# Performance work log

Measured on AMD Instinct MI355X. Metric: run time of the kernel, lower is better.

The kernel has to match this reference:

```python
import jax, jax.numpy as jnp
import numpy as np

B, T, C = 1, 2048, 1024
H, KVH = 16, 4
D = C // H            # 64
KV = KVH * D          # 256
EPS = 1e-6
SCALE = 1.0 / np.sqrt(D)
ROPE_BASE = 10000.0


def setup_inputs() -> dict:
    key = jax.random.key(0)
    ks = jax.random.split(key, 8)
    s = 0.02
    return dict(
        x=jax.random.normal(ks[0], (B, T, C), jnp.float32),
        Wq=jax.random.normal(ks[1], (C, C), jnp.float32) * s,
        Wk=jax.random.normal(ks[2], (KV, C), jnp.float32) * s,
        Wv=jax.random.normal(ks[3], (KV, C), jnp.float32) * s,
        Wo=jax.random.normal(ks[4], (C, C), jnp.float32) * s,
        q_norm_w=jnp.ones((C,), jnp.float32),
        k_norm_w=jnp.ones((KV,), jnp.float32),
        fgate_w=jax.random.normal(ks[5], (H, C), jnp.float32) * s,
        fgate_b=jnp.zeros((H,), jnp.float32),
        weight_lambda=jax.random.normal(ks[6], (C, H), jnp.float32) * s,
    )


def _rmsnorm(x, w):
    var = jnp.mean(x * x, axis=-1, keepdims=True)
    return x * jax.lax.rsqrt(var + EPS) * w


def _rotate_half(x):
    x1, x2 = jnp.split(x, 2, axis=-1)
    return jnp.concatenate([-x2, x1], axis=-1)


def _apply_rope(q, k):
    # q: [B,H,T,D], k: [B,KVH,T,D]; position_ids = arange(T)
    inv_freq = 1.0 / (ROPE_BASE ** (jnp.arange(0, D, 2, dtype=jnp.float32) / D))
    freqs = jnp.outer(jnp.arange(T, dtype=jnp.float32), inv_freq)  # [T, D/2]
    emb = jnp.concatenate([freqs, freqs], axis=-1)                 # [T, D]
    cos = jnp.cos(emb)[None, None]                                  # [1,1,T,D]
    sin = jnp.sin(emb)[None, None]
    return q * cos + _rotate_half(q) * sin, k * cos + _rotate_half(k) * sin


def _forward(x, Wq, Wk, Wv, Wo, q_norm_w, k_norm_w, fgate_w, fgate_b, weight_lambda):
    q = _rmsnorm(x @ Wq.T, q_norm_w)          # [B,T,C]
    k = _rmsnorm(x @ Wk.T, k_norm_w)          # [B,T,KV]
    v = x @ Wv.T                              # [B,T,KV]
    q = q.reshape(B, T, H, D).transpose(0, 2, 1, 3)     # [B,H,T,D]
    k = k.reshape(B, T, KVH, D).transpose(0, 2, 1, 3)   # [B,KVH,T,D]
    v = v.reshape(B, T, KVH, D).transpose(0, 2, 1, 3)
    q, k = _apply_rope(q, k)
    # GQA: repeat_interleave kv heads
    g = H // KVH
    k = jnp.repeat(k, g, axis=1)              # [B,H,T,D]
    v = jnp.repeat(v, g, axis=1)
    # Forgetting gate (FoX): log f_t per head, with elu-based lambda scaling
    lam = jax.nn.elu(x @ weight_lambda) + 1.0            # [B,T,H]
    logit = (x @ fgate_w.T + fgate_b) * lam              # [B,T,H]
    log_f = (jax.nn.log_sigmoid(logit) / (lam + 1e-3)).transpose(0, 2, 1)  # [B,H,T]
    c = jnp.cumsum(log_f, axis=-1)                       # [B,H,T]
    bias = c[..., :, None] - c[..., None, :]             # [B,H,T,T]: sum_{t=j+1..i} log f_t
    scores = jnp.einsum('bhid,bhjd->bhij', q, k) * SCALE + bias
    causal = jnp.tril(jnp.ones((T, T), dtype=bool))
    scores = jnp.where(causal, scores, -jnp.inf)
    p = jax.nn.softmax(scores, axis=-1)
    y = jnp.einsum('bhij,bhjd->bhid', p, v)              # [B,H,T,D]
    y = y.transpose(0, 2, 1, 3).reshape(B, T, C)
    return y @ Wo.T


def reference(x, Wq, Wk, Wv, Wo, q_norm_w, k_norm_w, fgate_w, fgate_b, weight_lambda):
    return _forward(x, Wq, Wk, Wv, Wo, q_norm_w, k_norm_w, fgate_w, fgate_b, weight_lambda)
```

## Files before the change

### kernel.cpp

```cpp
#include <hip/hip_runtime.h>

typedef __bf16 bf16x8 __attribute__((ext_vector_type(8)));
typedef float f32x4 __attribute__((ext_vector_type(4)));

#define MFMA_BF16 __builtin_amdgcn_mfma_f32_16x16x32_bf16

static constexpr int T_ = 2048;
static constexpr int C_ = 1024;
static constexpr int H_ = 16;
static constexpr int KVH_ = 4;
static constexpr int D_ = 64;
static constexpr float SCALE_ = 0.125f;
static constexpr float MSHIFT_ = 10.0f;

static constexpr int UPH_ = 528;
static constexpr int W_ = H_ * UPH_;
static constexpr int CHUNK_ = 12;
static constexpr int NBLK_ = W_ / CHUNK_;

__device__ inline void cvt8(__bf16* dst, const float* src) {
  float4 a = *(const float4*)src;
  float4 b = *(const float4*)(src + 4);
  bf16x8 r;
  r[0] = (__bf16)a.x; r[1] = (__bf16)a.y; r[2] = (__bf16)a.z; r[3] = (__bf16)a.w;
  r[4] = (__bf16)b.x; r[5] = (__bf16)b.y; r[6] = (__bf16)b.z; r[7] = (__bf16)b.w;
  *(bf16x8*)dst = r;
}

__global__ __launch_bounds__(256) void cvt_kernel(
    const float* __restrict__ x,  const float* __restrict__ wq,
    const float* __restrict__ wk, const float* __restrict__ wv,
    const float* __restrict__ wo, const float* __restrict__ wl,
    __bf16* __restrict__ xb,  __bf16* __restrict__ wqb,
    __bf16* __restrict__ wkb, __bf16* __restrict__ wvb,
    __bf16* __restrict__ wob, float* __restrict__ wlT,
    float* __restrict__ zbuf)
{
  size_t i8 = ((size_t)blockIdx.x * 256 + threadIdx.x) * 8;
  if (i8 < 2097152)       cvt8(xb  + i8,            x  + i8);
  else if (i8 < 3145728)  cvt8(wqb + (i8-2097152),  wq + (i8-2097152));
  else if (i8 < 3407872)  cvt8(wkb + (i8-3145728),  wk + (i8-3145728));
  else if (i8 < 3670016)  cvt8(wvb + (i8-3407872),  wv + (i8-3407872));
  else if (i8 < 4718592)  cvt8(wob + (i8-3670016),  wo + (i8-3670016));
  else if (i8 < 4734976) {
    size_t r = i8 - 4718592;
#pragma unroll
    for (int j = 0; j < 8; ++j) {
      size_t idx = r + j;
      size_t hh = idx >> 10, c = idx & 1023;
      wlT[idx] = wl[c * 16 + hh];
    }
  } else {
    size_t z = i8 - 4734976;
    if (z < 2129920) {
      float4 zz = {0.f, 0.f, 0.f, 0.f};
      *(float4*)(zbuf + z) = zz;
      *(float4*)(zbuf + z + 4) = zz;
    }
  }
}

template <int BM>
__global__ __launch_bounds__(256) void gemm_bt_kernel(
    const __bf16* __restrict__ A, int K, int N,
    const __bf16* __restrict__ B0, int e0,
    const __bf16* __restrict__ B1, int e1,
    const __bf16* __restrict__ B2,
    float* __restrict__ outF)
{
  __shared__ __bf16 la[BM * 40];
  __shared__ __bf16 lb[128 * 40];
  const int m0 = blockIdx.y * BM;
  const int n0 = blockIdx.x * 128;
  const __bf16* Bs; int nrel;
  if (n0 < e0)      { Bs = B0; nrel = n0; }
  else if (n0 < e1) { Bs = B1; nrel = n0 - e0; }
  else              { Bs = B2; nrel = n0 - e1; }
  const int tid = threadIdx.x;
  const int arow = tid >> 2, acol = (tid & 3) * 8;
  const __bf16* ap = A  + (size_t)(m0   + arow) * K + acol;
  const __bf16* bp = Bs + (size_t)(nrel + arow) * K + acol;
  const int w = tid >> 6, lane = tid & 63, lq = lane >> 4, ln = lane & 15;
  const int wm = (w >> 1) * (BM / 2), wn = (w & 1) * 64;
  constexpr int FM = BM / 32;
  f32x4 acc[FM][4] = {};
  for (int k0 = 0; k0 < K; k0 += 32) {
    bf16x8 a0 = *(const bf16x8*)(ap + k0);
    bf16x8 a1{};
    if (BM == 128) a1 = *(const bf16x8*)(ap + (size_t)64 * K + k0);
    bf16x8 b0 = *(const bf16x8*)(bp + k0);
    bf16x8 b1 = *(const bf16x8*)(bp + (size_t)64 * K + k0);
    __syncthreads();
    *(bf16x8*)(la + arow * 40 + acol) = a0;
    if (BM == 128) *(bf16x8*)(la + (arow + 64) * 40 + acol) = a1;
    *(bf16x8*)(lb + arow * 40 + acol) = b0;
    *(bf16x8*)(lb + (arow + 64) * 40 + acol) = b1;
    __syncthreads();
    bf16x8 af[FM], bfr[4];
#pragma unroll
    for (int i = 0; i < FM; ++i)
      af[i] = *(const bf16x8*)(la + (wm + i * 16 + ln) * 40 + lq * 8);
#pragma unroll
    for (int j = 0; j < 4; ++j)
      bfr[j] = *(const bf16x8*)(lb + (wn + j * 16 + ln) * 40 + lq * 8);
#pragma unroll
    for (int i = 0; i < FM; ++i)
#pragma unroll
      for (int j = 0; j < 4; ++j)
        acc[i][j] = MFMA_BF16(af[i], bfr[j], acc[i][j], 0, 0, 0);
  }
#pragma unroll
  for (int i = 0; i < FM; ++i)
#pragma unroll
    for (int j = 0; j < 4; ++j)
#pragma unroll
      for (int r = 0; r < 4; ++r) {
        int row = m0 + wm + i * 16 + lq * 4 + r;
        int col = n0 + wn + j * 16 + ln;
        outF[(size_t)row * N + col] = acc[i][j][r];
      }
}

__global__ __launch_bounds__(256) void gates_kernel(
    const float* __restrict__ x, const float* __restrict__ fw,
    const float* __restrict__ fb, const float* __restrict__ wlT,
    float* __restrict__ logf)
{
  const int t = blockIdx.x;
  const int tid = threadIdx.x, w = tid >> 6, lane = tid & 63;
  float xv[16];
#pragma unroll
  for (int i = 0; i < 16; ++i)
    xv[i] = x[(size_t)t * C_ + i * 64 + lane];
#pragma unroll
  for (int u = 0; u < 4; ++u) {
    int h = w * 4 + u;
    float s1 = 0.f, s2 = 0.f;
#pragma unroll
    for (int i = 0; i < 16; ++i) {
      int cidx = i * 64 + lane;
      s1 += xv[i] * wlT[(size_t)h * C_ + cidx];
      s2 += xv[i] * fw[(size_t)h * C_ + cidx];
    }
    for (int m = 32; m; m >>= 1) {
      s1 += __shfl_xor(s1, m);
      s2 += __shfl_xor(s2, m);
    }
    if (lane == 0) {
      float lam = (s1 > 0.f ? s1 : expm1f(s1)) + 1.0f;
      float logit = (s2 + fb[h]) * lam;
      float ls = (logit >= 0.f) ? -log1pf(expf(-logit))
                                : (logit - log1pf(expf(logit)));
      logf[(size_t)h * T_ + t] = ls / (lam + 1e-3f);
    }
  }
}

__global__ __launch_bounds__(64) void cumsum_kernel(
    const float* __restrict__ logf, float* __restrict__ csum)
{
  const int h = blockIdx.x;
  const int lane = threadIdx.x;
  float carry = 0.f;
  for (int ch = 0; ch < T_ / 64; ++ch) {
    float v = logf[(size_t)h * T_ + ch * 64 + lane];
#pragma unroll
    for (int d = 1; d < 64; d <<= 1) {
      float tv = __shfl_up(v, d);
      if (lane >= d) v += tv;
    }
    v += carry;
    csum[(size_t)h * T_ + ch * 64 + lane] = v;
    carry = __shfl(v, 63);
  }
}

__global__ __launch_bounds__(256) void normrope_kernel(
    const float* __restrict__ qkv, const float* __restrict__ qw,
    const float* __restrict__ kw, __bf16* __restrict__ qh,
    __bf16* __restrict__ kh, __bf16* __restrict__ vh)
{
  const int t = blockIdx.x, tid = threadIdx.x;
  __shared__ float qn[1024];
  __shared__ float kn[256];
  __shared__ float red[16];
  __shared__ float rc[32], rs[32];
  if (tid < 32) {
    float fr = (float)t * exp2f((float)tid * -0.41524101186404527f);
    float sn, cs;
    sincosf(fr, &sn, &cs);
    rc[tid] = cs; rs[tid] = sn;
  }
  const float* row = qkv + (size_t)t * 1536;
  float4 q4 = *(const float4*)(row + tid * 4);
  float kvl = row[1024 + tid];
  float vvl = row[1280 + tid];
  float ssq = q4.x * q4.x + q4.y * q4.y + q4.z * q4.z + q4.w * q4.w;
  float ssk = kvl * kvl;
  const int lane = tid & 63, w = tid >> 6;
  for (int m = 32; m; m >>= 1) {
    ssq += __shfl_xor(ssq, m);
    ssk += __shfl_xor(ssk, m);
  }
  if (lane == 0) { red[w] = ssq; red[8 + w] = ssk; }
  __syncthreads();
  float sq = red[0] + red[1] + red[2] + red[3];
  float sk = red[8] + red[9] + red[10] + red[11];
  float rq = rsqrtf(sq * (1.0f / 1024.f) + 1e-6f);
  float rk = rsqrtf(sk * (1.0f / 256.f) + 1e-6f);
  qn[tid * 4 + 0] = q4.x * rq * qw[tid * 4 + 0];
  qn[tid * 4 + 1] = q4.y * rq * qw[tid * 4 + 1];
  qn[tid * 4 + 2] = q4.z * rq * qw[tid * 4 + 2];
  qn[tid * 4 + 3] = q4.w * rq * qw[tid * 4 + 3];
  kn[tid] = kvl * rk * kw[tid];
  __syncthreads();
#pragma unroll
  for (int u = 0; u < 4; ++u) {
    int cidx = tid * 4 + u;
    int hh = cidx >> 6, d = cidx & 63, i = d & 31;
    float cs = rc[i], sn = rs[i];
    float val = (d < 32) ? (qn[cidx] * cs - qn[cidx + 32] * sn)
                         : (qn[cidx] * cs + qn[cidx - 32] * sn);
    qh[(size_t)hh * T_ * D_ + (size_t)t * D_ + d] = (__bf16)val;
  }
  {
    int d = tid & 63, kvhh = tid >> 6, i = d & 31;
    float cs = rc[i], sn = rs[i];
    float kval = (d < 32) ? (kn[tid] * cs - kn[tid + 32] * sn)
                          : (kn[tid] * cs + kn[tid - 32] * sn);
    kh[(size_t)kvhh * T_ * D_ + (size_t)t * D_ + d] = (__bf16)kval;
    vh[(size_t)kvhh * T_ * D_ + (size_t)t * D_ + d] = (__bf16)vvl;
  }
}

__global__ __launch_bounds__(256) void vtrans_kernel(
    const __bf16* __restrict__ vh, __bf16* __restrict__ vt)
{
  const int tb = blockIdx.x, kvh = blockIdx.y;
  __shared__ __bf16 tile[64][72];
  const int tid = threadIdx.x;
  const int r = tid >> 2, cb = (tid & 3) * 16;
  const __bf16* src = vh + (size_t)kvh * T_ * D_ + (size_t)(tb * 64 + r) * D_ + cb;
  bf16x8 v0 = *(const bf16x8*)(src);
  bf16x8 v1 = *(const bf16x8*)(src + 8);
  *(bf16x8*)(&tile[r][cb]) = v0;
  *(bf16x8*)(&tile[r][cb + 8]) = v1;
  __syncthreads();
  bf16x8 o0, o1;
#pragma unroll
  for (int j = 0; j < 8; ++j) o0[j] = tile[cb + j][r];
#pragma unroll
  for (int j = 0; j < 8; ++j) o1[j] = tile[cb + 8 + j][r];
  __bf16* dst = vt + (size_t)kvh * D_ * T_ + (size_t)r * T_ + tb * 64 + cb;
  *(bf16x8*)(dst) = o0;
  *(bf16x8*)(dst + 8) = o1;
}

__global__ __launch_bounds__(256) void attn_kernel(
    const __bf16* __restrict__ qh, const __bf16* __restrict__ kh,
    const __bf16* __restrict__ vt, const float* __restrict__ csum,
    float* __restrict__ oacc, float* __restrict__ lsacc)
{
  const int bid = blockIdx.x;
  const int wgid = (bid & 7) * (NBLK_ / 8) + (bid >> 3);
  const int u0 = wgid * CHUNK_;
  __shared__ __bf16 kbuf[2][64 * 72];
  __shared__ __bf16 vbuf[2][64 * 72];
  __shared__ __bf16 pt[4][16 * 76];
  const int tid = threadIdx.x;
  const int w = tid >> 6, lane = tid & 63, lq = lane >> 4, ln = lane & 15;
  const int srow = tid >> 2, scol = (tid & 3) * 16;
  bf16x8 ones;
#pragma unroll
  for (int j = 0; j < 8; ++j) ones[j] = (__bf16)1.0f;
  __bf16* pw = &pt[w][0];

  auto dec = [](int u, int& h, int& ib, int& jt) {
    h = u / UPH_;
    int uh = u - h * UPH_;
    int b = (int)((sqrtf((float)(8 * uh + 1)) - 1.f) * 0.5f);
    if (b * (b + 1) / 2 > uh) --b;
    if ((b + 1) * (b + 2) / 2 <= uh) ++b;
    ib = b; jt = uh - b * (b + 1) / 2;
  };

  int h, ib, jt;
  dec(u0, h, ib, jt);
  int kvh = h >> 2;

  bf16x8 aq0, aq1;
  float ci[4];
  f32x4 o[4] = {};
  f32x4 ls = {0.f, 0.f, 0.f, 0.f};
  auto loadQ = [&](int h_, int i0_) {
    const __bf16* qp = qh + ((size_t)h_ * T_ + i0_ + w * 16 + ln) * D_;
    aq0 = *(const bf16x8*)(qp + lq * 8);
    aq1 = *(const bf16x8*)(qp + 32 + lq * 8);
#pragma unroll
    for (int r = 0; r < 4; ++r)
      ci[r] = csum[(size_t)h_ * T_ + i0_ + w * 16 + lq * 4 + r];
#pragma unroll
    for (int dd = 0; dd < 4; ++dd) o[dd] = f32x4{0.f, 0.f, 0.f, 0.f};
    ls = f32x4{0.f, 0.f, 0.f, 0.f};
  };
  loadQ(h, ib * 64);

  auto fetchRegs = [&](int kvh_, int jt_, bf16x8& k0, bf16x8& k1,
                       bf16x8& v0, bf16x8& v1) {
    const __bf16* kb = kh + (size_t)kvh_ * T_ * D_;
    const __bf16* vb = vt + (size_t)kvh_ * D_ * T_;
    k0 = *(const bf16x8*)(kb + (size_t)(jt_ * 64 + srow) * D_ + scol);
    k1 = *(const bf16x8*)(kb + (size_t)(jt_ * 64 + srow) * D_ + scol + 8);
    v0 = *(const bf16x8*)(vb + (size_t)srow * T_ + jt_ * 64 + scol);
    v1 = *(const bf16x8*)(vb + (size_t)srow * T_ + jt_ * 64 + scol + 8);
  };
  auto writeStage = [&](int cb, bf16x8 k0, bf16x8 k1, bf16x8 v0, bf16x8 v1) {
    *(bf16x8*)(kbuf[cb] + srow * 72 + scol) = k0;
    *(bf16x8*)(kbuf[cb] + srow * 72 + scol + 8) = k1;
    *(bf16x8*)(vbuf[cb] + srow * 72 + scol) = v0;
    *(bf16x8*)(vbuf[cb] + srow * 72 + scol + 8) = v1;
  };

  auto tilebody = [&](int cb, int j0, bool diag) {
    const __bf16* kt = kbuf[cb];
    const __bf16* vtt = vbuf[cb];
    float cj[4];
#pragma unroll
    for (int jj = 0; jj < 4; ++jj)
      cj[jj] = csum[(size_t)h * T_ + j0 + jj * 16 + ln];
    f32x4 s[4];
    const f32x4 zf = {0.f, 0.f, 0.f, 0.f};
#pragma unroll
    for (int jj = 0; jj < 4; ++jj) {
      bf16x8 bk0 = *(const bf16x8*)(kt + (jj * 16 + ln) * 72 + lq * 8);
      bf16x8 bk1 = *(const bf16x8*)(kt + (jj * 16 + ln) * 72 + 32 + lq * 8);
      s[jj] = MFMA_BF16(aq0, bk0, zf, 0, 0, 0);
      s[jj] = MFMA_BF16(aq1, bk1, s[jj], 0, 0, 0);
    }
    bf16x8 bv0[4], bv1[4];
#pragma unroll
    for (int dd = 0; dd < 4; ++dd) {
      bv0[dd] = *(const bf16x8*)(vtt + (dd * 16 + ln) * 72 + lq * 8);
      bv1[dd] = *(const bf16x8*)(vtt + (dd * 16 + ln) * 72 + 32 + lq * 8);
    }
#pragma unroll
    for (int jj = 0; jj < 4; ++jj)
#pragma unroll
      for (int r = 0; r < 4; ++r) {
        float arg = fmaf(s[jj][r], SCALE_, ci[r] - cj[jj] - MSHIFT_);
        float p = __expf(arg);
        if (diag && (jj * 16 + ln > w * 16 + lq * 4 + r)) p = 0.f;
        pw[(lq * 4 + r) * 76 + jj * 16 + ln] = (__bf16)p;
      }
    asm volatile("s_waitcnt lgkmcnt(0)" ::: "memory");
    bf16x8 pa0 = *(const bf16x8*)(pw + ln * 76 + lq * 8);
    bf16x8 pa1 = *(const bf16x8*)(pw + ln * 76 + 32 + lq * 8);
    ls = MFMA_BF16(pa0, ones, ls, 0, 0, 0);
    ls = MFMA_BF16(pa1, ones, ls, 0, 0, 0);
#pragma unroll
    for (int dd = 0; dd < 4; ++dd) {
      o[dd] = MFMA_BF16(pa0, bv0[dd], o[dd], 0, 0, 0);
      o[dd] = MFMA_BF16(pa1, bv1[dd], o[dd], 0, 0, 0);
    }
  };

  auto flush = [&]() {
    const int i0 = ib * 64;
#pragma unroll
    for (int dd = 0; dd < 4; ++dd)
#pragma unroll
      for (int r = 0; r < 4; ++r) {
        int iabs = i0 + w * 16 + lq * 4 + r;
        atomicAdd(oacc + ((size_t)h * T_ + iabs) * D_ + dd * 16 + ln,
                  o[dd][r]);
      }
    if (ln == 0) {
#pragma unroll
      for (int r = 0; r < 4; ++r)
        atomicAdd(lsacc + (size_t)h * T_ + ib * 64 + w * 16 + lq * 4 + r,
                  ls[r]);
    }
  };

  {
    bf16x8 k0, k1, v0, v1;
    fetchRegs(kvh, jt, k0, k1, v0, v1);
    writeStage(0, k0, k1, v0, v1);
  }
  __syncthreads();

  int cur = 0;
#pragma unroll 1
  for (int s = 0; s < CHUNK_; ++s) {
    const bool last = (s == CHUNK_ - 1);
    int nh = 0, nib = 0, njt = 0;
    bf16x8 k0, k1, v0, v1;
    if (!last) {
      dec(u0 + s + 1, nh, nib, njt);
      fetchRegs(nh >> 2, njt, k0, k1, v0, v1);
    }
    tilebody(cur, jt * 64, jt == ib);
    if (!last) writeStage(cur ^ 1, k0, k1, v0, v1);
    const bool rowEnd = last || nib != ib || nh != h;
    if (rowEnd) flush();
    if (!last) {
      __syncthreads();
      if (nh != h || nib != ib) loadQ(nh, nib * 64);
      h = nh; ib = nib; jt = njt; kvh = nh >> 2;
      cur ^= 1;
    }
  }
}

__global__ __launch_bounds__(256) void attnfin_kernel(
    const float* __restrict__ oacc, const float* __restrict__ lsacc,
    __bf16* __restrict__ y)
{
  const int t = blockIdx.x;
  const int c = threadIdx.x * 4;
  const int h = c >> 6, d = c & 63;
  float inv = 1.0f / lsacc[(size_t)h * T_ + t];
  float4 o4 = *(const float4*)(oacc + ((size_t)h * T_ + t) * D_ + d);
  __bf16* yp = y + (size_t)t * C_ + c;
  yp[0] = (__bf16)(o4.x * inv);
  yp[1] = (__bf16)(o4.y * inv);
  yp[2] = (__bf16)(o4.z * inv);
  yp[3] = (__bf16)(o4.w * inv);
}

extern "C" void kernel_launch(void* const* d_in, const int* in_sizes, int n_in,
                              void* d_out, int out_size, void* d_ws, size_t ws_size,
                              hipStream_t stream) {
  const float* x   = (const float*)d_in[0];
  const float* Wq  = (const float*)d_in[1];
  const float* Wk  = (const float*)d_in[2];
  const float* Wv  = (const float*)d_in[3];
  const float* Wo  = (const float*)d_in[4];
  const float* qnw = (const float*)d_in[5];
  const float* knw = (const float*)d_in[6];
  const float* fgw = (const float*)d_in[7];
  const float* fgb = (const float*)d_in[8];
  const float* wl  = (const float*)d_in[9];

  char* ws = (char*)d_ws;
  size_t off = 0;
  float*  qkv  = (float*)(ws + off);  off += (size_t)T_ * 1536 * 4;
  float*  logf = (float*)(ws + off);  off += (size_t)H_ * T_ * 4;
  float*  csum = (float*)(ws + off);  off += (size_t)H_ * T_ * 4;
  __bf16* qh   = (__bf16*)(ws + off); off += (size_t)H_ * T_ * D_ * 2;
  __bf16* kh   = (__bf16*)(ws + off); off += (size_t)KVH_ * T_ * D_ * 2;
  __bf16* vh   = (__bf16*)(ws + off); off += (size_t)KVH_ * T_ * D_ * 2;
  __bf16* vt   = (__bf16*)(ws + off); off += (size_t)KVH_ * T_ * D_ * 2;
  __bf16* y    = (__bf16*)(ws + off); off += (size_t)T_ * C_ * 2;
  __bf16* xb   = (__bf16*)(ws + off); off += (size_t)T_ * C_ * 2;
  __bf16* wqb  = (__bf16*)(ws + off); off += (size_t)C_ * C_ * 2;
  __bf16* wkb  = (__bf16*)(ws + off); off += (size_t)256 * C_ * 2;
  __bf16* wvb  = (__bf16*)(ws + off); off += (size_t)256 * C_ * 2;
  __bf16* wob  = (__bf16*)(ws + off); off += (size_t)C_ * C_ * 2;
  float*  wlT  = (float*)(ws + off);  off += (size_t)H_ * C_ * 4;
  float*  oacc = (float*)(ws + off);  off += (size_t)H_ * T_ * D_ * 4;
  float*  lsacc= (float*)(ws + off);  off += (size_t)H_ * T_ * 4;

  cvt_kernel<<<3352, 256, 0, stream>>>(x, Wq, Wk, Wv, Wo, wl,
                                       xb, wqb, wkb, wvb, wob, wlT, oacc);
  gemm_bt_kernel<64><<<dim3(12, 32), 256, 0, stream>>>(
      xb, 1024, 1536, wqb, 1024, wkb, 1280, wvb, qkv);
  gates_kernel<<<T_, 256, 0, stream>>>(x, fgw, fgb, wlT, logf);
  cumsum_kernel<<<H_, 64, 0, stream>>>(logf, csum);
  normrope_kernel<<<T_, 256, 0, stream>>>(qkv, qnw, knw, qh, kh, vh);
  vtrans_kernel<<<dim3(T_ / 64, KVH_), 256, 0, stream>>>(vh, vt);
  attn_kernel<<<NBLK_, 256, 0, stream>>>(qh, kh, vt, csum, oacc, lsacc);
  attnfin_kernel<<<T_, 256, 0, stream>>>(oacc, lsacc, y);
  gemm_bt_kernel<64><<<dim3(8, 32), 256, 0, stream>>>(
      y, 1024, 1024, wob, 1024, wob, 1024, wob, (float*)d_out);
}
```

Before: 197.3 us.

## Fuse attention finalize into output GEMM, parallelize cumsum, tune attention kernel

Drops the separate attnfin kernel and bf16 y buffer by having a new output GEMM read the fp32 attention accumulators, normalize them by the row sums, and convert to bf16 while loading its A tile. The cumsum becomes a single-pass 256-thread block scan instead of a serial 64-lane loop over chunks. The attention kernel switches to exp2 with prescaled constants, reuses the idle K double-buffer for the P tile to cut LDS, adds launch bounds for occupancy and setprio around MFMAs, and shrinks CHUNK to 8 for more blocks. The GEMM A-load now reads fp32 oacc, which costs more bandwidth, and reusing the other K buffer for P relies on the timing of the next-stage write.

```diff
diff --git a/kernel.cpp b/kernel.cpp
--- a/kernel.cpp
+++ b/kernel.cpp
@@ -11,11 +11,13 @@
 static constexpr int KVH_ = 4;
 static constexpr int D_ = 64;
 static constexpr float SCALE_ = 0.125f;
+static constexpr float INVLN2_ = 1.4426950408889634f;
+static constexpr float SCALE2_ = 0.125f * 1.4426950408889634f;
 static constexpr float MSHIFT_ = 10.0f;
 
 static constexpr int UPH_ = 528;
 static constexpr int W_ = H_ * UPH_;
-static constexpr int CHUNK_ = 12;
+static constexpr int CHUNK_ = 8;
 static constexpr int NBLK_ = W_ / CHUNK_;
 
 __device__ inline void cvt8(__bf16* dst, const float* src) {
@@ -121,6 +123,66 @@
       }
 }
 
+__global__ __launch_bounds__(256) void gemmout_kernel(
+    const float* __restrict__ oacc, const float* __restrict__ lsacc,
+    const __bf16* __restrict__ B, float* __restrict__ outF)
+{
+  constexpr int K = 1024, N = 1024;
+  __shared__ __bf16 la[64 * 40];
+  __shared__ __bf16 lb[128 * 40];
+  const int m0 = blockIdx.y * 64;
+  const int n0 = blockIdx.x * 128;
+  const int tid = threadIdx.x;
+  const int arow = tid >> 2, acol = (tid & 3) * 8;
+  const int trow = m0 + arow;
+  const __bf16* bp = B + (size_t)(n0 + arow) * K + acol;
+  const int w = tid >> 6, lane = tid & 63, lq = lane >> 4, ln = lane & 15;
+  const int wm = (w >> 1) * 32, wn = (w & 1) * 64;
+  f32x4 acc[2][4] = {};
+  for (int k0 = 0; k0 < K; k0 += 32) {
+    const int c = k0 + acol;
+    const int hh = c >> 6, d = c & 63;
+    const float* op = oacc + ((size_t)hh * T_ + trow) * D_ + d;
+    float4 f0 = *(const float4*)(op);
+    float4 f1 = *(const float4*)(op + 4);
+    float inv = __builtin_amdgcn_rcpf(lsacc[(size_t)hh * T_ + trow]);
+    bf16x8 a0;
+    a0[0] = (__bf16)(f0.x * inv); a0[1] = (__bf16)(f0.y * inv);
+    a0[2] = (__bf16)(f0.z * inv); a0[3] = (__bf16)(f0.w * inv);
+    a0[4] = (__bf16)(f1.x * inv); a0[5] = (__bf16)(f1.y * inv);
+    a0[6] = (__bf16)(f1.z * inv); a0[7] = (__bf16)(f1.w * inv);
+    bf16x8 b0 = *(const bf16x8*)(bp + k0);
+    bf16x8 b1 = *(const bf16x8*)(bp + (size_t)64 * K + k0);
+    __syncthreads();
+    *(bf16x8*)(la + arow * 40 + acol) = a0;
+    *(bf16x8*)(lb + arow * 40 + acol) = b0;
+    *(bf16x8*)(lb + (arow + 64) * 40 + acol) = b1;
+    __syncthreads();
+    bf16x8 af[2], bfr[4];
+#pragma unroll
+    for (int i = 0; i < 2; ++i)
+      af[i] = *(const bf16x8*)(la + (wm + i * 16 + ln) * 40 + lq * 8);
+#pragma unroll
+    for (int j = 0; j < 4; ++j)
+      bfr[j] = *(const bf16x8*)(lb + (wn + j * 16 + ln) * 40 + lq * 8);
+#pragma unroll
+    for (int i = 0; i < 2; ++i)
+#pragma unroll
+      for (int j = 0; j < 4; ++j)
+        acc[i][j] = MFMA_BF16(af[i], bfr[j], acc[i][j], 0, 0, 0);
+  }
+#pragma unroll
+  for (int i = 0; i < 2; ++i)
+#pragma unroll
+    for (int j = 0; j < 4; ++j)
+#pragma unroll
+      for (int r = 0; r < 4; ++r) {
+        int row = m0 + wm + i * 16 + lq * 4 + r;
+        int col = n0 + wn + j * 16 + ln;
+        outF[(size_t)row * N + col] = acc[i][j][r];
+      }
+}
+
 __global__ __launch_bounds__(256) void gates_kernel(
     const float* __restrict__ x, const float* __restrict__ fw,
     const float* __restrict__ fb, const float* __restrict__ wlT,
@@ -156,23 +218,40 @@
   }
 }
 
-__global__ __launch_bounds__(64) void cumsum_kernel(
+__global__ __launch_bounds__(256) void cumsum_kernel(
     const float* __restrict__ logf, float* __restrict__ csum)
 {
   const int h = blockIdx.x;
-  const int lane = threadIdx.x;
-  float carry = 0.f;
-  for (int ch = 0; ch < T_ / 64; ++ch) {
-    float v = logf[(size_t)h * T_ + ch * 64 + lane];
-#pragma unroll
-    for (int d = 1; d < 64; d <<= 1) {
-      float tv = __shfl_up(v, d);
-      if (lane >= d) v += tv;
-    }
-    v += carry;
-    csum[(size_t)h * T_ + ch * 64 + lane] = v;
-    carry = __shfl(v, 63);
-  }
+  const int tid = threadIdx.x, lane = tid & 63, w = tid >> 6;
+  __shared__ float wsum[4];
+  const float* src = logf + (size_t)h * T_ + tid * 8;
+  float4 a = *(const float4*)(src);
+  float4 b = *(const float4*)(src + 4);
+  float v[8] = {a.x, a.y, a.z, a.w, b.x, b.y, b.z, b.w};
+  float t = 0.f;
+#pragma unroll
+  for (int j = 0; j < 8; ++j) t += v[j];
+  float s = t;
+#pragma unroll
+  for (int d = 1; d < 64; d <<= 1) {
+    float u = __shfl_up(s, d);
+    if (lane >= d) s += u;
+  }
+  if (lane == 63) wsum[w] = s;
+  __syncthreads();
+  float prefix = 0.f;
+#pragma unroll
+  for (int ww = 0; ww < 3; ++ww)
+    if (ww < w) prefix += wsum[ww];
+  float run = prefix + s - t;
+  float* dst = csum + (size_t)h * T_ + tid * 8;
+  float4 o0, o1;
+  run += v[0]; o0.x = run; run += v[1]; o0.y = run;
+  run += v[2]; o0.z = run; run += v[3]; o0.w = run;
+  run += v[4]; o1.x = run; run += v[5]; o1.y = run;
+  run += v[6]; o1.z = run; run += v[7]; o1.w = run;
+  *(float4*)dst = o0;
+  *(float4*)(dst + 4) = o1;
 }
 
 __global__ __launch_bounds__(256) void normrope_kernel(
@@ -256,7 +335,7 @@
   *(bf16x8*)(dst + 8) = o1;
 }
 
-__global__ __launch_bounds__(256) void attn_kernel(
+__global__ __launch_bounds__(256, 4) void attn_kernel(
     const __bf16* __restrict__ qh, const __bf16* __restrict__ kh,
     const __bf16* __restrict__ vt, const float* __restrict__ csum,
     float* __restrict__ oacc, float* __restrict__ lsacc)
@@ -266,14 +345,12 @@
   const int u0 = wgid * CHUNK_;
   __shared__ __bf16 kbuf[2][64 * 72];
   __shared__ __bf16 vbuf[2][64 * 72];
-  __shared__ __bf16 pt[4][16 * 76];
   const int tid = threadIdx.x;
   const int w = tid >> 6, lane = tid & 63, lq = lane >> 4, ln = lane & 15;
   const int srow = tid >> 2, scol = (tid & 3) * 16;
   bf16x8 ones;
 #pragma unroll
   for (int j = 0; j < 8; ++j) ones[j] = (__bf16)1.0f;
-  __bf16* pw = &pt[w][0];
 
   auto dec = [](int u, int& h, int& ib, int& jt) {
     h = u / UPH_;
@@ -289,7 +366,7 @@
   int kvh = h >> 2;
 
   bf16x8 aq0, aq1;
-  float ci[4];
+  float ci2[4];
   f32x4 o[4] = {};
   f32x4 ls = {0.f, 0.f, 0.f, 0.f};
   auto loadQ = [&](int h_, int i0_) {
@@ -298,7 +375,8 @@
     aq1 = *(const bf16x8*)(qp + 32 + lq * 8);
 #pragma unroll
     for (int r = 0; r < 4; ++r)
-      ci[r] = csum[(size_t)h_ * T_ + i0_ + w * 16 + lq * 4 + r];
+      ci2[r] = (csum[(size_t)h_ * T_ + i0_ + w * 16 + lq * 4 + r] - MSHIFT_)
+               * INVLN2_;
 #pragma unroll
     for (int dd = 0; dd < 4; ++dd) o[dd] = f32x4{0.f, 0.f, 0.f, 0.f};
     ls = f32x4{0.f, 0.f, 0.f, 0.f};
@@ -324,12 +402,14 @@
   auto tilebody = [&](int cb, int j0, bool diag) {
     const __bf16* kt = kbuf[cb];
     const __bf16* vtt = vbuf[cb];
-    float cj[4];
+    __bf16* pw = kbuf[cb ^ 1] + w * 16 * 72;
+    float cj2[4];
 #pragma unroll
     for (int jj = 0; jj < 4; ++jj)
-      cj[jj] = csum[(size_t)h * T_ + j0 + jj * 16 + ln];
+      cj2[jj] = csum[(size_t)h * T_ + j0 + jj * 16 + ln] * INVLN2_;
     f32x4 s[4];
     const f32x4 zf = {0.f, 0.f, 0.f, 0.f};
+    __builtin_amdgcn_s_setprio(1);
 #pragma unroll
     for (int jj = 0; jj < 4; ++jj) {
       bf16x8 bk0 = *(const bf16x8*)(kt + (jj * 16 + ln) * 72 + lq * 8);
@@ -337,6 +417,7 @@
       s[jj] = MFMA_BF16(aq0, bk0, zf, 0, 0, 0);
       s[jj] = MFMA_BF16(aq1, bk1, s[jj], 0, 0, 0);
     }
+    __builtin_amdgcn_s_setprio(0);
     bf16x8 bv0[4], bv1[4];
 #pragma unroll
     for (int dd = 0; dd < 4; ++dd) {
@@ -347,14 +428,15 @@
     for (int jj = 0; jj < 4; ++jj)
 #pragma unroll
       for (int r = 0; r < 4; ++r) {
-        float arg = fmaf(s[jj][r], SCALE_, ci[r] - cj[jj] - MSHIFT_);
-        float p = __expf(arg);
+        float arg = fmaf(s[jj][r], SCALE2_, ci2[r] - cj2[jj]);
+        float p = exp2f(arg);
         if (diag && (jj * 16 + ln > w * 16 + lq * 4 + r)) p = 0.f;
-        pw[(lq * 4 + r) * 76 + jj * 16 + ln] = (__bf16)p;
+        pw[(lq * 4 + r) * 72 + jj * 16 + ln] = (__bf16)p;
       }
     asm volatile("s_waitcnt lgkmcnt(0)" ::: "memory");
-    bf16x8 pa0 = *(const bf16x8*)(pw + ln * 76 + lq * 8);
-    bf16x8 pa1 = *(const bf16x8*)(pw + ln * 76 + 32 + lq * 8);
+    bf16x8 pa0 = *(const bf16x8*)(pw + ln * 72 + lq * 8);
+    bf16x8 pa1 = *(const bf16x8*)(pw + ln * 72 + 32 + lq * 8);
+    __builtin_amdgcn_s_setprio(1);
     ls = MFMA_BF16(pa0, ones, ls, 0, 0, 0);
     ls = MFMA_BF16(pa1, ones, ls, 0, 0, 0);
 #pragma unroll
@@ -362,6 +444,7 @@
       o[dd] = MFMA_BF16(pa0, bv0[dd], o[dd], 0, 0, 0);
       o[dd] = MFMA_BF16(pa1, bv1[dd], o[dd], 0, 0, 0);
     }
+    __builtin_amdgcn_s_setprio(0);
   };
 
   auto flush = [&]() {
@@ -410,22 +493,6 @@
       cur ^= 1;
     }
   }
-}
-
-__global__ __launch_bounds__(256) void attnfin_kernel(
-    const float* __restrict__ oacc, const float* __restrict__ lsacc,
-    __bf16* __restrict__ y)
-{
-  const int t = blockIdx.x;
-  const int c = threadIdx.x * 4;
-  const int h = c >> 6, d = c & 63;
-  float inv = 1.0f / lsacc[(size_t)h * T_ + t];
-  float4 o4 = *(const float4*)(oacc + ((size_t)h * T_ + t) * D_ + d);
-  __bf16* yp = y + (size_t)t * C_ + c;
-  yp[0] = (__bf16)(o4.x * inv);
-  yp[1] = (__bf16)(o4.y * inv);
-  yp[2] = (__bf16)(o4.z * inv);
-  yp[3] = (__bf16)(o4.w * inv);
 }
 
 extern "C" void kernel_launch(void* const* d_in, const int* in_sizes, int n_in,
@@ -451,7 +518,6 @@
   __bf16* kh   = (__bf16*)(ws + off); off += (size_t)KVH_ * T_ * D_ * 2;
   __bf16* vh   = (__bf16*)(ws + off); off += (size_t)KVH_ * T_ * D_ * 2;
   __bf16* vt   = (__bf16*)(ws + off); off += (size_t)KVH_ * T_ * D_ * 2;
-  __bf16* y    = (__bf16*)(ws + off); off += (size_t)T_ * C_ * 2;
   __bf16* xb   = (__bf16*)(ws + off); off += (size_t)T_ * C_ * 2;
   __bf16* wqb  = (__bf16*)(ws + off); off += (size_t)C_ * C_ * 2;
   __bf16* wkb  = (__bf16*)(ws + off); off += (size_t)256 * C_ * 2;
@@ -466,11 +532,10 @@
   gemm_bt_kernel<64><<<dim3(12, 32), 256, 0, stream>>>(
       xb, 1024, 1536, wqb, 1024, wkb, 1280, wvb, qkv);
   gates_kernel<<<T_, 256, 0, stream>>>(x, fgw, fgb, wlT, logf);
-  cumsum_kernel<<<H_, 64, 0, stream>>>(logf, csum);
+  cumsum_kernel<<<H_, 256, 0, stream>>>(logf, csum);
   normrope_kernel<<<T_, 256, 0, stream>>>(qkv, qnw, knw, qh, kh, vh);
   vtrans_kernel<<<dim3(T_ / 64, KVH_), 256, 0, stream>>>(vh, vt);
   attn_kernel<<<NBLK_, 256, 0, stream>>>(qh, kh, vt, csum, oacc, lsacc);
-  attnfin_kernel<<<T_, 256, 0, stream>>>(oacc, lsacc, y);
-  gemm_bt_kernel<64><<<dim3(8, 32), 256, 0, stream>>>(
-      y, 1024, 1024, wob, 1024, wob, 1024, wob, (float*)d_out);
-}
+  gemmout_kernel<<<dim3(8, 32), 256, 0, stream>>>(
+      oacc, lsacc, wob, (float*)d_out);
+}
```

Measured after the change: 194.4 us. About the same (-1.5%).
